# Kernel optimization log

Measured on AMD Instinct MI355X. Metric: run time of the kernel, lower is better.

## Reference

```python
import jax, jax.numpy as jnp
import numpy as np

INPUT_DIM = 1024
DAY_EMB = 8
PRED_LEN = 96
HIDDEN = 512
BATCH = 4096


def setup_inputs() -> dict:
    key = jax.random.key(0)
    ks = jax.random.split(key, 6)
    x = jax.random.normal(ks[0], (BATCH, INPUT_DIM), dtype=jnp.float32)
    day_emb = jax.random.normal(ks[1], (PRED_LEN, DAY_EMB), dtype=jnp.float32)
    # stacked per-head first-layer weights: in = input_dim + day_emb_dim
    W1 = jax.random.normal(ks[2], (PRED_LEN, INPUT_DIM + DAY_EMB, HIDDEN), dtype=jnp.float32) * 0.02
    b1 = jax.random.normal(ks[3], (PRED_LEN, HIDDEN), dtype=jnp.float32) * 0.02
    # stacked per-head output Linear(hidden, 1) weights (squeezed)
    W2 = jax.random.normal(ks[4], (PRED_LEN, HIDDEN), dtype=jnp.float32) * 0.02
    b2 = jax.random.normal(ks[5], (PRED_LEN,), dtype=jnp.float32) * 0.02
    return {"x": x, "day_emb": day_emb, "W1": W1, "b1": b1, "W2": W2, "b2": b2}


def reference(x, day_emb, W1, b1, W2, b2):
    # Each head p sees f = concat([x, day_emb[p]]) -> Linear -> ReLU -> (Dropout eval=id) -> Linear(.,1)
    # Split W1 into the x-part and emb-part so we never materialize the [P,B,in+emb] concat.
    W1x = W1[:, :INPUT_DIM, :]          # [P, D, H]
    W1e = W1[:, INPUT_DIM:, :]          # [P, E, H]
    h = jnp.einsum('bd,pdh->pbh', x, W1x)  # [P, B, H]
    h = h + (jnp.einsum('pe,peh->ph', day_emb, W1e) + b1)[:, None, :]
    h = jax.nn.relu(h)
    out = jnp.einsum('pbh,ph->pb', h, W2) + b2[:, None]  # [P, B]
    return out.T  # [B, pred_len]
```

## Files before the change

kernel.cpp:

```cpp
#include <hip/hip_runtime.h>
#include <hip/hip_bf16.h>
#include <stdint.h>

#define INPUT_DIM 1024
#define PRED_LEN 96
#define HIDDEN 512
#define BATCH 4096
#define W1_ROWS 1032

typedef __attribute__((ext_vector_type(8))) short bf16x8;
typedef __attribute__((ext_vector_type(4))) float floatx4;

__device__ __forceinline__ unsigned short f32_to_bf16_rne(float f) {
    union { float f; unsigned int u; } v; v.f = f;
    unsigned int u = v.u;
    unsigned int r = u + 0x7fffu + ((u >> 16) & 1u);
    return (unsigned short)(r >> 16);
}

__device__ __forceinline__ unsigned int pack_bf16x2(float lo, float hi) {
    return (unsigned int)f32_to_bf16_rne(lo) | ((unsigned int)f32_to_bf16_rne(hi) << 16);
}

__device__ __forceinline__ void async_copy16(const void* g, void* l) {
    __builtin_amdgcn_global_load_lds(
        (const __attribute__((address_space(1))) unsigned int*)g,
        (__attribute__((address_space(3))) unsigned int*)l, 16, 0, 0);
}

#define TP_BLOCKS  (PRED_LEN * 8 * 4)
#define CV_BLOCKS  ((BATCH * INPUT_DIM) / (256 * 8))
__global__ void __launch_bounds__(256) prep_kernel(
        const float* __restrict__ x,
        const float* __restrict__ W1,
        const float* __restrict__ day_emb,
        const float* __restrict__ b1,
        unsigned short* __restrict__ xb,
        unsigned short* __restrict__ W1t,
        float* __restrict__ bias) {
    const int bid = blockIdx.x;
    const int t   = threadIdx.x;

    if (bid < TP_BLOCKS) {
        const int nt = bid & 7;
        const int kt = (bid >> 3) & 3;
        const int p  = bid >> 5;
        const int tn = t & 15;
        const int tk = t >> 4;
        const int n0 = nt * 64;
        const int k0 = kt * 256;

        const float* src = W1 + (size_t)p * W1_ROWS * HIDDEN
                              + (size_t)(k0 + 16 * tk) * HIDDEN + n0 + 4 * tn;
        float4 v[16];
        #pragma unroll
        for (int i = 0; i < 16; ++i)
            v[i] = *reinterpret_cast<const float4*>(src + (size_t)i * HIDDEN);

        size_t dst = ((size_t)p * HIDDEN + n0 + 4 * tn) * 1024 + k0 + 16 * tk;
        #pragma unroll
        for (int j = 0; j < 4; ++j) {
            float c[16];
            #pragma unroll
            for (int i = 0; i < 16; ++i)
                c[i] = (j == 0) ? v[i].x : (j == 1) ? v[i].y : (j == 2) ? v[i].z : v[i].w;
            uint4 o0, o1;
            o0.x = pack_bf16x2(c[0],  c[1]);
            o0.y = pack_bf16x2(c[2],  c[3]);
            o0.z = pack_bf16x2(c[4],  c[5]);
            o0.w = pack_bf16x2(c[6],  c[7]);
            o1.x = pack_bf16x2(c[8],  c[9]);
            o1.y = pack_bf16x2(c[10], c[11]);
            o1.z = pack_bf16x2(c[12], c[13]);
            o1.w = pack_bf16x2(c[14], c[15]);
            unsigned short* d = W1t + dst + (size_t)j * 1024;
            *reinterpret_cast<uint4*>(d)     = o0;
            *reinterpret_cast<uint4*>(d + 8) = o1;
        }
    } else if (bid < TP_BLOCKS + CV_BLOCKS) {
        const int b = bid - TP_BLOCKS;
        const int i = (b * 256 + t) * 8;
        float4 a = *reinterpret_cast<const float4*>(x + i);
        float4 c = *reinterpret_cast<const float4*>(x + i + 4);
        uint4 o;
        o.x = pack_bf16x2(a.x, a.y);
        o.y = pack_bf16x2(a.z, a.w);
        o.z = pack_bf16x2(c.x, c.y);
        o.w = pack_bf16x2(c.z, c.w);
        *reinterpret_cast<uint4*>(xb + i) = o;
    } else {
        const int p = bid - (TP_BLOCKS + CV_BLOCKS);
        const float* W1e = W1 + ((size_t)p * W1_ROWS + INPUT_DIM) * HIDDEN;
        #pragma unroll
        for (int s = 0; s < 2; ++s) {
            const int h = t + s * 256;
            float acc = b1[p * HIDDEN + h];
            #pragma unroll
            for (int e = 0; e < 8; ++e)
                acc += day_emb[p * 8 + e] * W1e[(size_t)e * HIDDEN + h];
            bias[p * HIDDEN + h] = acc;
        }
    }
}

__global__ void __launch_bounds__(256, 2)
mlp_head_kernel(const unsigned short* __restrict__ xb,
                const unsigned short* __restrict__ W1t,
                const float* __restrict__ bias,
                const float* __restrict__ W2,
                const float* __restrict__ b2,
                float* __restrict__ out)
{
    __shared__ unsigned short As[128 * 64];
    __shared__ unsigned short Bs[256 * 64];
    __shared__ float w2s[HIDDEN];
    __shared__ float biass[HIDDEN];

    const int mt   = blockIdx.x;
    const int p    = blockIdx.y;
    const int t    = threadIdx.x;
    const int lane = t & 63;
    const int w    = t >> 6;
    const int wi   = w >> 1;
    const int wj   = w & 1;
    const int l15  = lane & 15;
    const int quad = lane >> 4;
    const int xl   = l15 & 7;

    const int t3    = t >> 3;
    const int skc   = ((t & 7) ^ (t3 & 7)) * 8;
    const int ldsq8 = t * 8;

    for (int i = t; i < HIDDEN; i += 256) {
        w2s[i]   = W2[p * HIDDEN + i];
        biass[i] = bias[p * HIDDEN + i];
    }

    const int m0 = mt * 128;
    const unsigned short* ag = xb  + (size_t)m0 * 1024 + (size_t)t3 * 1024 + skc;
    const unsigned short* bg = W1t + (size_t)p * HIDDEN * 1024 + (size_t)t3 * 1024 + skc;

    float partial[4][4];
    #pragma unroll
    for (int i = 0; i < 4; ++i)
        #pragma unroll
        for (int r = 0; r < 4; ++r) partial[i][r] = 0.f;

    floatx4 acc[4][8];
    #pragma unroll
    for (int i = 0; i < 4; ++i)
        #pragma unroll
        for (int j = 0; j < 8; ++j)
            acc[i][j] = (floatx4){0.f, 0.f, 0.f, 0.f};

    #pragma unroll 1
    for (int vk = 0; vk < 32; ++vk) {
        const int k0 = (vk & 15) << 6;
        const size_t bnn = (size_t)(vk >> 4) * 262144;

        __syncthreads();
        #pragma unroll
        for (int c = 0; c < 4; ++c)
            async_copy16(ag + (size_t)c * 32768 + k0, As + ldsq8 + c * 2048);
        #pragma unroll
        for (int c = 0; c < 8; ++c)
            async_copy16(bg + bnn + (size_t)c * 32768 + k0, Bs + ldsq8 + c * 2048);
        __syncthreads();

        #pragma unroll
        for (int kk = 0; kk < 2; ++kk) {
            const int slot = (kk * 4 + quad) ^ xl;
            bf16x8 af[4], bfr[8];
            #pragma unroll
            for (int i = 0; i < 4; ++i) {
                int r = wi * 64 + i * 16 + l15;
                af[i] = *reinterpret_cast<const bf16x8*>(As + r * 64 + slot * 8);
            }
            #pragma unroll
            for (int j = 0; j < 8; ++j) {
                int n = wj * 128 + j * 16 + l15;
                bfr[j] = *reinterpret_cast<const bf16x8*>(Bs + n * 64 + slot * 8);
            }
            #pragma unroll
            for (int i = 0; i < 4; ++i)
                #pragma unroll
                for (int j = 0; j < 8; ++j)
                    acc[i][j] = __builtin_amdgcn_mfma_f32_16x16x32_bf16(
                        af[i], bfr[j], acc[i][j], 0, 0, 0);
        }

        if ((vk & 15) == 15) {
            const int n0 = (vk >> 4) * 256;
            #pragma unroll
            for (int j = 0; j < 8; ++j) {
                int c = n0 + wj * 128 + j * 16 + l15;
                float w2v = w2s[c];
                float bv  = biass[c];
                #pragma unroll
                for (int i = 0; i < 4; ++i)
                    #pragma unroll
                    for (int r = 0; r < 4; ++r) {
                        float hv = acc[i][j][r] + bv;
                        hv = hv > 0.f ? hv : 0.f;
                        partial[i][r] += hv * w2v;
                        acc[i][j][r] = 0.f;
                    }
            }
        }
    }

    #pragma unroll
    for (int i = 0; i < 4; ++i)
        #pragma unroll
        for (int r = 0; r < 4; ++r) {
            float v = partial[i][r];
            v += __shfl_xor(v, 1);
            v += __shfl_xor(v, 2);
            v += __shfl_xor(v, 4);
            v += __shfl_xor(v, 8);
            partial[i][r] = v;
        }

    __syncthreads();
    float* red = reinterpret_cast<float*>(As);

    if (l15 == 0) {
        #pragma unroll
        for (int i = 0; i < 4; ++i)
            #pragma unroll
            for (int r = 0; r < 4; ++r) {
                int row = wi * 64 + i * 16 + quad * 4 + r;
                red[wj * 128 + row] = partial[i][r];
            }
    }
    __syncthreads();
    if (t < 128) {
        float v = red[t] + red[128 + t] + b2[p];
        out[(size_t)(m0 + t) * PRED_LEN + p] = v;
    }
}

extern "C" void kernel_launch(void* const* d_in, const int* in_sizes, int n_in,
                              void* d_out, int out_size, void* d_ws, size_t ws_size,
                              hipStream_t stream) {
    const float* x       = (const float*)d_in[0];
    const float* day_emb = (const float*)d_in[1];
    const float* W1      = (const float*)d_in[2];
    const float* b1      = (const float*)d_in[3];
    const float* W2      = (const float*)d_in[4];
    const float* b2      = (const float*)d_in[5];
    float* out = (float*)d_out;

    const size_t xb_bytes  = (size_t)BATCH * INPUT_DIM * 2;
    const size_t w1t_bytes = (size_t)PRED_LEN * HIDDEN * INPUT_DIM * 2;
    const size_t bias_bytes = (size_t)PRED_LEN * HIDDEN * 4;
    if (ws_size < xb_bytes + w1t_bytes + bias_bytes) return;

    unsigned short* xb  = (unsigned short*)d_ws;
    unsigned short* w1t = (unsigned short*)((char*)d_ws + xb_bytes);
    float* biasp        = (float*)((char*)d_ws + xb_bytes + w1t_bytes);

    prep_kernel<<<TP_BLOCKS + CV_BLOCKS + PRED_LEN, 256, 0, stream>>>(
        x, W1, day_emb, b1, xb, w1t, biasp);

    dim3 grid(BATCH / 128, PRED_LEN);
    mlp_head_kernel<<<grid, 256, 0, stream>>>(xb, w1t, biasp, W2, b2, out);
}
```

Measured before the change: 645.0 us.

## Double-buffer B tile and prefetch next K-slice during MFMA compute

```diff
diff --git a/kernel.cpp b/kernel.cpp
--- a/kernel.cpp
+++ b/kernel.cpp
@@ -112,9 +112,7 @@
                 float* __restrict__ out)
 {
     __shared__ unsigned short As[128 * 64];
-    __shared__ unsigned short Bs[256 * 64];
-    __shared__ float w2s[HIDDEN];
-    __shared__ float biass[HIDDEN];
+    __shared__ unsigned short Bs[2][256 * 64];
 
     const int mt   = blockIdx.x;
     const int p    = blockIdx.y;
@@ -131,10 +129,15 @@
     const int skc   = ((t & 7) ^ (t3 & 7)) * 8;
     const int ldsq8 = t * 8;
 
-    for (int i = t; i < HIDDEN; i += 256) {
-        w2s[i]   = W2[p * HIDDEN + i];
-        biass[i] = bias[p * HIDDEN + i];
-    }
+    float w2r[16], br[16];
+    #pragma unroll
+    for (int nt2 = 0; nt2 < 2; ++nt2)
+        #pragma unroll
+        for (int j = 0; j < 8; ++j) {
+            int c = nt2 * 256 + wj * 128 + j * 16 + l15;
+            w2r[nt2 * 8 + j] = W2[p * HIDDEN + c];
+            br[nt2 * 8 + j]  = bias[p * HIDDEN + c];
+        }
 
     const int m0 = mt * 128;
     const unsigned short* ag = xb  + (size_t)m0 * 1024 + (size_t)t3 * 1024 + skc;
@@ -153,49 +156,66 @@
         for (int j = 0; j < 8; ++j)
             acc[i][j] = (floatx4){0.f, 0.f, 0.f, 0.f};
 
+    #pragma unroll
+    for (int c = 0; c < 4; ++c)
+        async_copy16(ag + (size_t)c * 32768, As + ldsq8 + c * 2048);
+    #pragma unroll
+    for (int c = 0; c < 8; ++c)
+        async_copy16(bg + (size_t)c * 32768, &Bs[0][ldsq8 + c * 2048]);
+    __syncthreads();
+
     #pragma unroll 1
     for (int vk = 0; vk < 32; ++vk) {
-        const int k0 = (vk & 15) << 6;
-        const size_t bnn = (size_t)(vk >> 4) * 262144;
-
-        __syncthreads();
-        #pragma unroll
-        for (int c = 0; c < 4; ++c)
-            async_copy16(ag + (size_t)c * 32768 + k0, As + ldsq8 + c * 2048);
-        #pragma unroll
-        for (int c = 0; c < 8; ++c)
-            async_copy16(bg + bnn + (size_t)c * 32768 + k0, Bs + ldsq8 + c * 2048);
-        __syncthreads();
-
+        const int cur = vk & 1;
+
+        bf16x8 afr[2][4];
         #pragma unroll
         for (int kk = 0; kk < 2; ++kk) {
             const int slot = (kk * 4 + quad) ^ xl;
-            bf16x8 af[4], bfr[8];
             #pragma unroll
             for (int i = 0; i < 4; ++i) {
                 int r = wi * 64 + i * 16 + l15;
-                af[i] = *reinterpret_cast<const bf16x8*>(As + r * 64 + slot * 8);
-            }
+                afr[kk][i] = *reinterpret_cast<const bf16x8*>(As + r * 64 + slot * 8);
+            }
+        }
+        __syncthreads();
+
+        if (vk < 31) {
+            const int nvk    = vk + 1;
+            const int k0n    = (nvk & 15) << 6;
+            const size_t bnn = (size_t)(nvk >> 4) * 262144;
+            #pragma unroll
+            for (int c = 0; c < 4; ++c)
+                async_copy16(ag + (size_t)c * 32768 + k0n, As + ldsq8 + c * 2048);
+            #pragma unroll
+            for (int c = 0; c < 8; ++c)
+                async_copy16(bg + bnn + (size_t)c * 32768 + k0n,
+                             &Bs[cur ^ 1][ldsq8 + c * 2048]);
+        }
+
+        const unsigned short* Bb = &Bs[cur][0];
+        #pragma unroll
+        for (int kk = 0; kk < 2; ++kk) {
+            const int slot = (kk * 4 + quad) ^ xl;
+            bf16x8 bfr[8];
             #pragma unroll
             for (int j = 0; j < 8; ++j) {
                 int n = wj * 128 + j * 16 + l15;
-                bfr[j] = *reinterpret_cast<const bf16x8*>(Bs + n * 64 + slot * 8);
+                bfr[j] = *reinterpret_cast<const bf16x8*>(Bb + n * 64 + slot * 8);
             }
             #pragma unroll
             for (int i = 0; i < 4; ++i)
                 #pragma unroll
                 for (int j = 0; j < 8; ++j)
                     acc[i][j] = __builtin_amdgcn_mfma_f32_16x16x32_bf16(
-                        af[i], bfr[j], acc[i][j], 0, 0, 0);
-        }
-
-        if ((vk & 15) == 15) {
-            const int n0 = (vk >> 4) * 256;
+                        afr[kk][i], bfr[j], acc[i][j], 0, 0, 0);
+        }
+
+        if (vk == 15) {
             #pragma unroll
             for (int j = 0; j < 8; ++j) {
-                int c = n0 + wj * 128 + j * 16 + l15;
-                float w2v = w2s[c];
-                float bv  = biass[c];
+                float w2v = w2r[j];
+                float bv  = br[j];
                 #pragma unroll
                 for (int i = 0; i < 4; ++i)
                     #pragma unroll
@@ -206,7 +226,23 @@
                         acc[i][j][r] = 0.f;
                     }
             }
-        }
+        } else if (vk == 31) {
+            #pragma unroll
+            for (int j = 0; j < 8; ++j) {
+                float w2v = w2r[8 + j];
+                float bv  = br[8 + j];
+                #pragma unroll
+                for (int i = 0; i < 4; ++i)
+                    #pragma unroll
+                    for (int r = 0; r < 4; ++r) {
+                        float hv = acc[i][j][r] + bv;
+                        hv = hv > 0.f ? hv : 0.f;
+                        partial[i][r] += hv * w2v;
+                    }
+            }
+        }
+
+        __syncthreads();
     }
 
     #pragma unroll
@@ -221,7 +257,6 @@
             partial[i][r] = v;
         }
 
-    __syncthreads();
     float* red = reinterpret_cast<float*>(As);
 
     if (l15 == 0) {
```

Result: slower. 737.4 us (+14.3%).
